# Optimization experiments

Measured on AMD Instinct MI355X. Metric: run time of the kernel, lower is better.

## Reference

```python
import jax, jax.numpy as jnp
import numpy as np


def setup_inputs() -> dict:
    key = jax.random.key(0)
    k1, k2 = jax.random.split(key)
    N, M, D = 8192, 8192, 3
    pred = jax.random.normal(k1, (N, D), dtype=jnp.float32)
    label = jax.random.normal(k2, (M, D), dtype=jnp.float32)
    return {"pred": pred, "label": label}


def reference(pred, label):
    # pairwise L2 distances: dis[n, m] = ||pred[n] - label[m]||_2
    diff = pred[:, None, :] - label[None, :, :]        # [N, M, D]
    dis = jnp.sqrt(jnp.sum(diff * diff, axis=2))       # [N, M]
    dis_xy = jnp.mean(jnp.min(dis, axis=1))            # for each x, nearest y
    dis_yx = jnp.mean(jnp.min(dis, axis=0))            # for each y, nearest x
    return dis_xy + dis_yx
```

## Files before the change

kernel.cpp:

```cpp
#include <hip/hip_runtime.h>
#include <math.h>

#define TPB 256
#define QPT 4
#define CH  64
#define CSR 128

__global__ __launch_bounds__(TPB) void pairmin_kernel(
    const float* __restrict__ pred, const float* __restrict__ label,
    float* __restrict__ part, int N, int M) {
  const int dir = blockIdx.z;
  const float* __restrict__ q = dir ? label : pred;
  const float* __restrict__ r = dir ? pred : label;
  const int nq = dir ? M : N;
  const int nr = dir ? N : M;
  const int cs = nr / CH;

  __shared__ float s[CSR * 3];
  const int t = threadIdx.x;
  if (t < (cs * 3) / 4)
    ((float4*)s)[t] = ((const float4*)(r + (size_t)blockIdx.y * cs * 3))[t];
  __syncthreads();

  const int i0 = (blockIdx.x * TPB + t) * QPT;
  const float4 Q0 = *(const float4*)(q + (size_t)i0 * 3 + 0);
  const float4 Q1 = *(const float4*)(q + (size_t)i0 * 3 + 4);
  const float4 Q2 = *(const float4*)(q + (size_t)i0 * 3 + 8);
  const float px[QPT] = {Q0.x, Q0.w, Q1.z, Q2.y};
  const float py[QPT] = {Q0.y, Q1.x, Q1.w, Q2.z};
  const float pz[QPT] = {Q0.z, Q1.y, Q2.x, Q2.w};

  float m[QPT] = {3.4e38f, 3.4e38f, 3.4e38f, 3.4e38f};

#pragma unroll 2
  for (int j = 0; j < cs / 4; ++j) {
    const float4 A = ((const float4*)s)[3 * j + 0];
    const float4 B = ((const float4*)s)[3 * j + 1];
    const float4 C = ((const float4*)s)[3 * j + 2];
    const float rx[4] = {A.x, A.w, B.z, C.y};
    const float ry[4] = {A.y, B.x, B.w, C.z};
    const float rz[4] = {A.z, B.y, C.x, C.w};
#pragma unroll
    for (int rr = 0; rr < 4; ++rr) {
#pragma unroll
      for (int qq = 0; qq < QPT; ++qq) {
        const float dx = px[qq] - rx[rr];
        const float dy = py[qq] - ry[rr];
        const float dz = pz[qq] - rz[rr];
        const float d = dx * dx + dy * dy + dz * dz;
        m[qq] = fminf(m[qq], d);
      }
    }
  }

  const size_t off = dir ? (size_t)CH * (size_t)N : 0;
  *(float4*)&part[off + (size_t)blockIdx.y * nq + i0] =
      make_float4(m[0], m[1], m[2], m[3]);
}

__global__ __launch_bounds__(TPB) void reduce_kernel(
    const float* __restrict__ part, float* __restrict__ bsums, int N, int M) {
  const int nbx = N / TPB;
  const int b = blockIdx.x;
  const int dir = (b >= nbx) ? 1 : 0;
  const int pb = dir ? (b - nbx) : b;
  const int nq = dir ? M : N;
  const size_t off = dir ? (size_t)CH * (size_t)N : 0;
  const int t = threadIdx.x;
  const int i = pb * TPB + t;

  float m = 3.4e38f;
#pragma unroll
  for (int c = 0; c < CH; ++c)
    m = fminf(m, part[off + (size_t)c * nq + i]);
  float d = sqrtf(m);

  for (int o = 32; o >= 1; o >>= 1) d += __shfl_down(d, o);
  __shared__ float wsum[TPB / 64];
  if ((t & 63) == 0) wsum[t >> 6] = d;
  __syncthreads();
  if (t == 0) {
    float sum = 0.f;
#pragma unroll
    for (int w = 0; w < TPB / 64; ++w) sum += wsum[w];
    bsums[b] = sum;
  }
}

__global__ void final_kernel(const float* __restrict__ bsums,
                             float* __restrict__ out,
                             int nbx, int nby, int N, int M) {
  const int t = threadIdx.x;
  float v0 = (t < nbx) ? bsums[t] : 0.0f;
  float v1 = (t < nby) ? bsums[nbx + t] : 0.0f;
  for (int o = 32; o >= 1; o >>= 1) {
    v0 += __shfl_down(v0, o);
    v1 += __shfl_down(v1, o);
  }
  if (t == 0) out[0] = v0 / (float)N + v1 / (float)M;
}

extern "C" void kernel_launch(void* const* d_in, const int* in_sizes, int n_in,
                              void* d_out, int out_size, void* d_ws, size_t ws_size,
                              hipStream_t stream) {
  const float* pred  = (const float*)d_in[0];
  const float* label = (const float*)d_in[1];
  const int N = in_sizes[0] / 3;
  const int M = in_sizes[1] / 3;

  float* part  = (float*)d_ws;
  float* bsums = part + (size_t)CH * (size_t)(N + M);

  const int nbx = N / TPB;
  const int nby = M / TPB;

  pairmin_kernel<<<dim3(N / (TPB * QPT), CH, 2), TPB, 0, stream>>>(
      pred, label, part, N, M);
  reduce_kernel<<<nbx + nby, TPB, 0, stream>>>(part, bsums, N, M);
  final_kernel<<<1, 64, 0, stream>>>(bsums, (float*)d_out, nbx, nby, N, M);
}
```

Measured before the change: 81.81 us.

## Use dot-product expansion for nearest-neighbor distances and double queries per thread

Rewrites the squared distance as |q|^2 - 2(q·r - |r|^2/2). Each inner pair now takes three FMAs plus a max instead of three subtracts, three multiply-adds and a min. Reference points are stored in shared memory as float4 with a precomputed half-norm, and the |q|^2 term is added back in the reduce kernel before the sqrt. Queries per thread go from 4 to 8, which halves the x-grid and raises register use. The expanded form can lose precision through cancellation, which the clamp to zero only partly covers.

```diff
diff --git a/kernel.cpp b/kernel.cpp
--- a/kernel.cpp
+++ b/kernel.cpp
@@ -2,7 +2,7 @@
 #include <math.h>
 
 #define TPB 256
-#define QPT 4
+#define QPT 8
 #define CH  64
 #define CSR 128
 
@@ -16,64 +16,78 @@
   const int nr = dir ? N : M;
   const int cs = nr / CH;
 
-  __shared__ float s[CSR * 3];
+  __shared__ float4 s[CSR];
   const int t = threadIdx.x;
-  if (t < (cs * 3) / 4)
-    ((float4*)s)[t] = ((const float4*)(r + (size_t)blockIdx.y * cs * 3))[t];
+  if (t < cs) {
+    const float* rp = r + ((size_t)blockIdx.y * cs + t) * 3;
+    const float rx = rp[0], ry = rp[1], rz = rp[2];
+    s[t] = make_float4(rx, ry, rz, 0.5f * (rx * rx + ry * ry + rz * rz));
+  }
   __syncthreads();
 
   const int i0 = (blockIdx.x * TPB + t) * QPT;
-  const float4 Q0 = *(const float4*)(q + (size_t)i0 * 3 + 0);
-  const float4 Q1 = *(const float4*)(q + (size_t)i0 * 3 + 4);
-  const float4 Q2 = *(const float4*)(q + (size_t)i0 * 3 + 8);
-  const float px[QPT] = {Q0.x, Q0.w, Q1.z, Q2.y};
-  const float py[QPT] = {Q0.y, Q1.x, Q1.w, Q2.z};
-  const float pz[QPT] = {Q0.z, Q1.y, Q2.x, Q2.w};
-
-  float m[QPT] = {3.4e38f, 3.4e38f, 3.4e38f, 3.4e38f};
+  float px[QPT], py[QPT], pz[QPT], m[QPT];
+  {
+    const float4* qv = (const float4*)(q + (size_t)i0 * 3);
+    float c[24];
+#pragma unroll
+    for (int v = 0; v < 6; ++v) {
+      float4 f = qv[v];
+      c[4 * v + 0] = f.x; c[4 * v + 1] = f.y; c[4 * v + 2] = f.z; c[4 * v + 3] = f.w;
+    }
+#pragma unroll
+    for (int qq = 0; qq < QPT; ++qq) {
+      px[qq] = c[3 * qq + 0];
+      py[qq] = c[3 * qq + 1];
+      pz[qq] = c[3 * qq + 2];
+      m[qq] = -3.4e38f;
+    }
+  }
 
 #pragma unroll 2
   for (int j = 0; j < cs / 4; ++j) {
-    const float4 A = ((const float4*)s)[3 * j + 0];
-    const float4 B = ((const float4*)s)[3 * j + 1];
-    const float4 C = ((const float4*)s)[3 * j + 2];
-    const float rx[4] = {A.x, A.w, B.z, C.y};
-    const float ry[4] = {A.y, B.x, B.w, C.z};
-    const float rz[4] = {A.z, B.y, C.x, C.w};
+    float4 R[4];
+#pragma unroll
+    for (int rr = 0; rr < 4; ++rr) R[rr] = s[4 * j + rr];
 #pragma unroll
     for (int rr = 0; rr < 4; ++rr) {
 #pragma unroll
       for (int qq = 0; qq < QPT; ++qq) {
-        const float dx = px[qq] - rx[rr];
-        const float dy = py[qq] - ry[rr];
-        const float dz = pz[qq] - rz[rr];
-        const float d = dx * dx + dy * dy + dz * dz;
-        m[qq] = fminf(m[qq], d);
+        float v = fmaf(pz[qq], R[rr].z, -R[rr].w);
+        v = fmaf(py[qq], R[rr].y, v);
+        v = fmaf(px[qq], R[rr].x, v);
+        m[qq] = fmaxf(m[qq], v);
       }
     }
   }
 
   const size_t off = dir ? (size_t)CH * (size_t)N : 0;
-  *(float4*)&part[off + (size_t)blockIdx.y * nq + i0] =
-      make_float4(m[0], m[1], m[2], m[3]);
+  float* dst = &part[off + (size_t)blockIdx.y * nq + i0];
+  *(float4*)(dst + 0) = make_float4(m[0], m[1], m[2], m[3]);
+  *(float4*)(dst + 4) = make_float4(m[4], m[5], m[6], m[7]);
 }
 
 __global__ __launch_bounds__(TPB) void reduce_kernel(
+    const float* __restrict__ pred, const float* __restrict__ label,
     const float* __restrict__ part, float* __restrict__ bsums, int N, int M) {
   const int nbx = N / TPB;
   const int b = blockIdx.x;
   const int dir = (b >= nbx) ? 1 : 0;
   const int pb = dir ? (b - nbx) : b;
   const int nq = dir ? M : N;
+  const float* __restrict__ q = dir ? label : pred;
   const size_t off = dir ? (size_t)CH * (size_t)N : 0;
   const int t = threadIdx.x;
   const int i = pb * TPB + t;
 
-  float m = 3.4e38f;
+  float m = -3.4e38f;
 #pragma unroll
   for (int c = 0; c < CH; ++c)
-    m = fminf(m, part[off + (size_t)c * nq + i]);
-  float d = sqrtf(m);
+    m = fmaxf(m, part[off + (size_t)c * nq + i]);
+
+  const float qx = q[3 * i + 0], qy = q[3 * i + 1], qz = q[3 * i + 2];
+  const float pp = qx * qx + qy * qy + qz * qz;
+  float d = sqrtf(fmaxf(0.0f, fmaf(-2.0f, m, pp)));
 
   for (int o = 32; o >= 1; o >>= 1) d += __shfl_down(d, o);
   __shared__ float wsum[TPB / 64];
@@ -116,6 +130,6 @@
 
   pairmin_kernel<<<dim3(N / (TPB * QPT), CH, 2), TPB, 0, stream>>>(
       pred, label, part, N, M);
-  reduce_kernel<<<nbx + nby, TPB, 0, stream>>>(part, bsums, N, M);
+  reduce_kernel<<<nbx + nby, TPB, 0, stream>>>(pred, label, part, bsums, N, M);
   final_kernel<<<1, 64, 0, stream>>>(bsums, (float*)d_out, nbx, nby, N, M);
 }
```

Measured after the change: 69.75 us (median of 2 runs). -14.7%, faster.
